# Kernel tuning notes

Hardware: AMD Instinct MI355X
Metric: run time of the kernel (lower is better)

The kernel has to match this reference:

```python
import jax, jax.numpy as jnp
import numpy as np
from jax import lax

EPS = 1e-5
DW_THRESH = 4.0
PW_THRESH = 1e-3


def setup_inputs() -> dict:
    key = jax.random.key(0)
    ks = jax.random.split(key, 13)
    B, C, O, H, W = 32, 256, 256, 56, 56
    inp = {
        "x": jax.random.normal(ks[0], (B, C, H, W), jnp.float32),
        "dw_w": jax.random.normal(ks[1], (C, 1, 3, 3), jnp.float32) * 0.2,
        "dw_b": jax.random.normal(ks[2], (C,), jnp.float32) * 0.1,
        "bn1_gamma": 0.5 + jax.random.uniform(ks[3], (C,), jnp.float32) * 1.5,
        "bn1_beta": jax.random.normal(ks[4], (C,), jnp.float32) * 0.5,
        "bn1_mean": jax.random.normal(ks[5], (C,), jnp.float32) * 0.1,
        "bn1_var": 0.5 + jax.random.uniform(ks[6], (C,), jnp.float32),
        "pw_w": jax.random.normal(ks[7], (O, C, 1, 1), jnp.float32) * 0.06,
        "pw_b": jax.random.normal(ks[8], (O,), jnp.float32) * 0.1,
        "bn2_gamma": 0.5 + jax.random.uniform(ks[9], (O,), jnp.float32) * 1.5,
        "bn2_beta": jax.random.normal(ks[10], (O,), jnp.float32) * 0.5,
        "bn2_mean": jax.random.normal(ks[11], (O,), jnp.float32) * 0.1,
        "bn2_var": 0.5 + jax.random.uniform(ks[12], (O,), jnp.float32),
    }
    return inp


def _bn(x, gamma, beta, mean, var):
    # inference-mode BatchNorm2d over channel axis 1
    inv = gamma * lax.rsqrt(var + EPS)
    return x * inv[None, :, None, None] + (beta - mean * inv)[None, :, None, None]


def _cut(x, thresh):
    # per-(batch, channel) max-abs pruning: max(max(x), -min(x)) == max(|x|)
    max_abs = jnp.max(jnp.abs(x), axis=(2, 3))  # [B, C]
    return jnp.where((max_abs < thresh)[:, :, None, None], 0.0, x)


def reference(x, dw_w, dw_b, bn1_gamma, bn1_beta, bn1_mean, bn1_var,
              pw_w, pw_b, bn2_gamma, bn2_beta, bn2_mean, bn2_var):
    C = x.shape[1]
    # depthwise 3x3 conv, padding=1, groups=C
    y = lax.conv_general_dilated(
        x, dw_w, window_strides=(1, 1), padding=[(1, 1), (1, 1)],
        feature_group_count=C,
        dimension_numbers=("NCHW", "OIHW", "NCHW"),
    ) + dw_b[None, :, None, None]
    y = jax.nn.relu(_bn(y, bn1_gamma, bn1_beta, bn1_mean, bn1_var))
    y = _cut(y, DW_THRESH)
    # pointwise 1x1 conv as channel contraction
    z = jnp.einsum("bihw,oi->bohw", y, pw_w[:, :, 0, 0]) + pw_b[None, :, None, None]
    z = jax.nn.relu(_bn(z, bn2_gamma, bn2_beta, bn2_mean, bn2_var))
    z = _cut(z, PW_THRESH)
    return z
```

## Files before the change

### kernel.cpp

```cpp
#include <hip/hip_runtime.h>
#include <hip/hip_bf16.h>
#include <stdint.h>

#define BATCH 32
#define CIN   256
#define COUT  256
#define HW    3136
#define NPAD  3200

typedef short bf16x8 __attribute__((ext_vector_type(8)));
typedef float f32x4  __attribute__((ext_vector_type(4)));

__device__ __forceinline__ unsigned short f2bf(float f) {
    unsigned u = __float_as_uint(f);
    u += 0x7fffu + ((u >> 16) & 1u);
    return (unsigned short)(u >> 16);
}

__global__ __launch_bounds__(256) void prep_kernel(
        const float* __restrict__ pw_w, const float* __restrict__ pw_b,
        const float* __restrict__ g2, const float* __restrict__ be2,
        const float* __restrict__ mu2, const float* __restrict__ va2,
        unsigned short* __restrict__ Wp, float* __restrict__ b2,
        unsigned* __restrict__ pwmax) {
    int o = blockIdx.x;
    int t = threadIdx.x;
    float inv2 = g2[o] * rsqrtf(va2[o] + 1e-5f);
    Wp[o * CIN + t] = f2bf(pw_w[o * CIN + t] * inv2);
    if (t == 0) b2[o] = pw_b[o] * inv2 + be2[o] - mu2[o] * inv2;
    int idx = blockIdx.x * 256 + t;
    if (idx < BATCH * COUT) pwmax[idx] = 0u;
}

#define LOADROW(dst, rp, mrow) do {                                        \
    float4 v0_ = *(const float4*)((rp) + c0);                              \
    float4 v1_ = *(const float4*)((rp) + c0 + 4);                          \
    dst[0] = (rp)[lidx] * (msL * (mrow));                                  \
    dst[1] = v0_.x * (mrow); dst[2] = v0_.y * (mrow);                      \
    dst[3] = v0_.z * (mrow); dst[4] = v0_.w * (mrow);                      \
    dst[5] = v1_.x * (mrow); dst[6] = v1_.y * (mrow);                      \
    dst[7] = v1_.z * (mrow); dst[8] = v1_.w * (mrow);                      \
    dst[9] = (rp)[ridx] * (msR * (mrow));                                  \
} while (0)

__global__ __launch_bounds__(256, 3) void dw_kernel(
        const float* __restrict__ x, const float* __restrict__ dww,
        const float* __restrict__ dwb,
        const float* __restrict__ g1, const float* __restrict__ be1,
        const float* __restrict__ mu1, const float* __restrict__ va1,
        unsigned short* __restrict__ y, float* __restrict__ dwmax) {
    int tid = threadIdx.x;
    int blk = blockIdx.x;
    __shared__ float lmx[256];

    float lmax = 0.f;
    if (tid < 224) {
        int p    = tid / 28;
        int r28  = tid - p * 28;
        int band = r28 / 7;
        int sc   = r28 - band * 7;
        int plane = blk * 8 + p;
        int c = plane & 255;
        int r0 = band * 14;
        int c0 = sc * 8;

        const float* xq = x + (size_t)plane * HW;
        float w00 = dww[c*9+0], w01 = dww[c*9+1], w02 = dww[c*9+2];
        float w10 = dww[c*9+3], w11 = dww[c*9+4], w12 = dww[c*9+5];
        float w20 = dww[c*9+6], w21 = dww[c*9+7], w22 = dww[c*9+8];
        float inv = g1[c] * rsqrtf(va1[c] + 1e-5f);
        float b0  = dwb[c] * inv + (be1[c] - mu1[c] * inv);

        float msL  = (sc == 0) ? 0.f : 1.f;
        float msR  = (sc == 6) ? 0.f : 1.f;
        int   lidx = (sc == 0) ? c0 : c0 - 1;
        int   ridx = (sc == 6) ? c0 + 7 : c0 + 8;
        float mTop = (band == 0) ? 0.f : 1.f;
        float mBot = (band == 3) ? 0.f : 1.f;

        float A[10], Bv[10], Cv[10], nx[10];
        {
            const float* rp = xq + ((band == 0) ? 0 : (r0 - 1)) * 56;
            LOADROW(A, rp, mTop);
        }
        {
            const float* rp = xq + r0 * 56;
            LOADROW(Bv, rp, 1.f);
        }
        {
            const float* rp = xq + (r0 + 1) * 56;
            LOADROW(nx, rp, 1.f);
        }
        unsigned short* yq = y + (size_t)plane * NPAD + c0;

#pragma unroll
        for (int i = 0; i < 14; ++i) {
#pragma unroll
            for (int t2 = 0; t2 < 10; ++t2) Cv[t2] = nx[t2];
            if (i < 13) {
                const float* rp = xq + ((i == 12) ? ((band == 3) ? 55 : (r0 + 14))
                                                  : (r0 + i + 2)) * 56;
                if (i == 12) { LOADROW(nx, rp, mBot); }
                else         { LOADROW(nx, rp, 1.f); }
            }
            unsigned us[8];
#pragma unroll
            for (int j = 0; j < 8; ++j) {
                float o = fmaf(A[j],    w00, fmaf(A[j+1],  w01, fmaf(A[j+2],  w02,
                          fmaf(Bv[j],   w10, fmaf(Bv[j+1], w11, fmaf(Bv[j+2], w12,
                          fmaf(Cv[j],   w20, fmaf(Cv[j+1], w21, Cv[j+2] * w22))))))));
                float v = fmaxf(fmaf(o, inv, b0), 0.f);
                lmax = fmaxf(lmax, v);
                us[j] = f2bf(v);
            }
            uint4 st;
            st.x = us[0] | (us[1] << 16);
            st.y = us[2] | (us[3] << 16);
            st.z = us[4] | (us[5] << 16);
            st.w = us[6] | (us[7] << 16);
            *(uint4*)(yq + (r0 + i) * 56) = st;
#pragma unroll
            for (int t2 = 0; t2 < 10; ++t2) { A[t2] = Bv[t2]; Bv[t2] = Cv[t2]; }
        }
    }
    lmx[tid] = lmax;
    __syncthreads();
    if (tid < 8) {
        float m = 0.f;
#pragma unroll 4
        for (int j = 0; j < 28; ++j) m = fmaxf(m, lmx[tid * 28 + j]);
        dwmax[blk * 8 + tid] = m;
    }
    if (tid < 64) {
        int p = tid >> 3;
        uint4* dst = (uint4*)(y + (size_t)(blk * 8 + p) * NPAD + HW) + (tid & 7);
        *dst = make_uint4(0, 0, 0, 0);
    }
}

__global__ __launch_bounds__(256) void pw_kernel(
        const unsigned short* __restrict__ y, const unsigned short* __restrict__ Wp,
        const float* __restrict__ b2, const float* __restrict__ dwm,
        float* __restrict__ z, unsigned* __restrict__ pwmax) {
    __shared__ __align__(16) unsigned short Al[128 * 64];
    __shared__ __align__(16) unsigned short Bl[128 * 64];

    int bid0 = blockIdx.x;
    int bid = (bid0 & 7) * 200 + (bid0 >> 3);
    int mt = bid & 1;
    int rest = bid >> 1;
    int nt = rest % 25;
    int b = rest / 25;
    int m0 = mt * 128, n0 = nt * 128;

    int tid = threadIdx.x;
    int lane = tid & 63, wid = tid >> 6;
    int wm = (wid & 1) * 64, wn = (wid >> 1) * 64;
    int l15 = lane & 15, l4 = lane >> 4;

    const unsigned short* yb = y + (size_t)b * CIN * NPAD;
    const float* dwb_ = dwm + b * 256;

    int am[4], acch[4];
    const unsigned short* asrc[4];
#pragma unroll
    for (int i = 0; i < 4; ++i) {
        int s = i * 256 + tid;
        int m = s >> 3, cch = s & 7, dch = cch ^ (m & 7);
        am[i] = m; acch[i] = cch;
        asrc[i] = Wp + (size_t)(m0 + m) * CIN + dch * 8;
    }
    int bq[2], bnq[2];
    const unsigned short* bsrc[2];
#pragma unroll
    for (int i = 0; i < 2; ++i) {
        int u = tid + i * 256;
        bq[i] = u >> 5; bnq[i] = u & 31;
        bsrc[i] = yb + (size_t)(bq[i] * 4) * NPAD + n0 + bnq[i] * 4;
    }

    uint4 areg[4];
    uint2 breg[2][4];
    float4 fl[2];
#pragma unroll
    for (int i = 0; i < 4; ++i) areg[i] = *(const uint4*)(asrc[i]);
#pragma unroll
    for (int i = 0; i < 2; ++i) {
#pragma unroll
        for (int r = 0; r < 4; ++r) breg[i][r] = *(const uint2*)(bsrc[i] + r * NPAD);
        fl[i] = *(const float4*)(dwb_ + bq[i] * 4);
    }

    f32x4 acc[4][4];
#pragma unroll
    for (int mf = 0; mf < 4; ++mf)
#pragma unroll
        for (int nf = 0; nf < 4; ++nf) acc[mf][nf] = {0.f, 0.f, 0.f, 0.f};

#pragma unroll
    for (int kk = 0; kk < 4; ++kk) {
        __builtin_amdgcn_s_barrier();
        __builtin_amdgcn_sched_barrier(0);
#pragma unroll
        for (int i = 0; i < 4; ++i)
            *(uint4*)((char*)Al + am[i] * 128 + acch[i] * 16) = areg[i];
#pragma unroll
        for (int i = 0; i < 2; ++i) {
            unsigned mk0 = fl[i].x >= 4.0f ? 0xffffffffu : 0u;
            unsigned mk1 = fl[i].y >= 4.0f ? 0xffffffffu : 0u;
            unsigned mk2 = fl[i].z >= 4.0f ? 0xffffffffu : 0u;
            unsigned mk3 = fl[i].w >= 4.0f ? 0xffffffffu : 0u;
            uint2 r0 = breg[i][0], r1 = breg[i][1], r2 = breg[i][2], r3 = breg[i][3];
            r0.x &= mk0; r0.y &= mk0; r1.x &= mk1; r1.y &= mk1;
            r2.x &= mk2; r2.y &= mk2; r3.x &= mk3; r3.y &= mk3;
            int q = bq[i], nq = bnq[i];
#pragma unroll
            for (int i2 = 0; i2 < 4; ++i2) {
                unsigned x0 = (i2 & 2) ? r0.y : r0.x;
                unsigned x1 = (i2 & 2) ? r1.y : r1.x;
                unsigned x2 = (i2 & 2) ? r2.y : r2.x;
                unsigned x3 = (i2 & 2) ? r3.y : r3.x;
                if (i2 & 1) { x0 >>= 16; x2 >>= 16; }
                else        { x0 &= 0xffffu; x2 &= 0xffffu; }
                unsigned px = (i2 & 1) ? (x0 | (x1 & 0xffff0000u))
                                       : (x0 | (x1 << 16));
                unsigned py = (i2 & 1) ? (x2 | (x3 & 0xffff0000u))
                                       : (x2 | (x3 << 16));
                int nloc = nq * 4 + i2;
                int sb = nloc * 128 + (((q >> 1) ^ ((nloc >> 2) & 7)) << 4) + ((q & 1) << 3);
                *(uint2*)((char*)Bl + sb) = make_uint2(px, py);
            }
        }
        if (kk < 3) {
#pragma unroll
            for (int i = 0; i < 4; ++i)
                areg[i] = *(const uint4*)(asrc[i] + (kk + 1) * 64);
#pragma unroll
            for (int i = 0; i < 2; ++i) {
#pragma unroll
                for (int r = 0; r < 4; ++r)
                    breg[i][r] = *(const uint2*)(bsrc[i] + (size_t)(kk + 1) * 64 * NPAD + r * NPAD);
                fl[i] = *(const float4*)(dwb_ + (kk + 1) * 64 + bq[i] * 4);
            }
        }
        asm volatile("s_waitcnt lgkmcnt(0)" ::: "memory");
        __builtin_amdgcn_s_barrier();
        __builtin_amdgcn_sched_barrier(0);
#pragma unroll
        for (int h = 0; h < 2; ++h) {
            bf16x8 af[4], bfr[4];
            int cc = h * 4 + l4;
#pragma unroll
            for (int mf = 0; mf < 4; ++mf) {
                int m = wm + mf * 16 + l15;
                af[mf] = *(const bf16x8*)((const char*)Al + m * 128 + ((cc ^ (m & 7)) << 4));
            }
#pragma unroll
            for (int nf = 0; nf < 4; ++nf) {
                int n = wn + nf * 16 + l15;
                bfr[nf] = *(const bf16x8*)((const char*)Bl + n * 128 + ((cc ^ ((n >> 2) & 7)) << 4));
            }
#pragma unroll
            for (int mf = 0; mf < 4; ++mf)
#pragma unroll
                for (int nf = 0; nf < 4; ++nf)
                    acc[mf][nf] = __builtin_amdgcn_mfma_f32_16x16x32_bf16(
                        af[mf], bfr[nf], acc[mf][nf], 0, 0, 0);
        }
    }

    float* zb = z + (size_t)b * COUT * HW;
#pragma unroll
    for (int mf = 0; mf < 4; ++mf) {
        int obase = m0 + wm + mf * 16 + l4 * 4;
        float bb0 = b2[obase + 0], bb1 = b2[obase + 1];
        float bb2v = b2[obase + 2], bb3 = b2[obase + 3];
        float rmax[4] = {0.f, 0.f, 0.f, 0.f};
#pragma unroll
        for (int nf = 0; nf < 4; ++nf) {
            int n = n0 + wn + nf * 16 + l15;
            bool valid = (n < HW);
            float v0 = fmaxf(acc[mf][nf][0] + bb0, 0.f);
            float v1 = fmaxf(acc[mf][nf][1] + bb1, 0.f);
            float v2 = fmaxf(acc[mf][nf][2] + bb2v, 0.f);
            float v3 = fmaxf(acc[mf][nf][3] + bb3, 0.f);
            if (valid) {
                zb[(size_t)(obase + 0) * HW + n] = v0;
                zb[(size_t)(obase + 1) * HW + n] = v1;
                zb[(size_t)(obase + 2) * HW + n] = v2;
                zb[(size_t)(obase + 3) * HW + n] = v3;
                rmax[0] = fmaxf(rmax[0], v0);
                rmax[1] = fmaxf(rmax[1], v1);
                rmax[2] = fmaxf(rmax[2], v2);
                rmax[3] = fmaxf(rmax[3], v3);
            }
        }
#pragma unroll
        for (int r = 0; r < 4; ++r) {
            float v = rmax[r];
            v = fmaxf(v, __shfl_xor(v, 1, 64));
            v = fmaxf(v, __shfl_xor(v, 2, 64));
            v = fmaxf(v, __shfl_xor(v, 4, 64));
            v = fmaxf(v, __shfl_xor(v, 8, 64));
            if (l15 == 0)
                atomicMax(&pwmax[b * COUT + obase + r], __float_as_uint(v));
        }
    }
}

__global__ __launch_bounds__(256) void cut_kernel(const unsigned* __restrict__ pwmax,
                                                  float* __restrict__ z) {
    int base = blockIdx.x * 8;
#pragma unroll
    for (int j = 0; j < 8; ++j) {
        int bo = base + j;
        if (__uint_as_float(pwmax[bo]) >= 1e-3f) continue;
        float4* zp = (float4*)(z + (size_t)bo * HW);
        for (int i = threadIdx.x; i < HW / 4; i += 256)
            zp[i] = make_float4(0.f, 0.f, 0.f, 0.f);
    }
}

extern "C" void kernel_launch(void* const* d_in, const int* in_sizes, int n_in,
                              void* d_out, int out_size, void* d_ws, size_t ws_size,
                              hipStream_t stream) {
    const float* x   = (const float*)d_in[0];
    const float* dww = (const float*)d_in[1];
    const float* dwb = (const float*)d_in[2];
    const float* g1  = (const float*)d_in[3];
    const float* be1 = (const float*)d_in[4];
    const float* mu1 = (const float*)d_in[5];
    const float* va1 = (const float*)d_in[6];
    const float* pww = (const float*)d_in[7];
    const float* pwb = (const float*)d_in[8];
    const float* g2  = (const float*)d_in[9];
    const float* be2 = (const float*)d_in[10];
    const float* mu2 = (const float*)d_in[11];
    const float* va2 = (const float*)d_in[12];
    float* z = (float*)d_out;

    char* ws = (char*)d_ws;
    const size_t Y_BYTES = (size_t)BATCH * CIN * NPAD * 2;
    unsigned short* y  = (unsigned short*)ws;
    unsigned short* Wp = (unsigned short*)(ws + Y_BYTES);
    float* b2          = (float*)(ws + Y_BYTES + 131072);
    unsigned* pwmax    = (unsigned*)(ws + Y_BYTES + 131072 + 1024);
    float* dwmax       = (float*)(ws + Y_BYTES + 131072 + 1024 + 32768);

    prep_kernel<<<256, 256, 0, stream>>>(pww, pwb, g2, be2, mu2, va2, Wp, b2, pwmax);
    dw_kernel<<<1024, 256, 0, stream>>>(x, dww, dwb, g1, be1, mu1, va1, y, dwmax);
    pw_kernel<<<1600, 256, 0, stream>>>(y, Wp, b2, dwmax, z, pwmax);
    cut_kernel<<<BATCH * COUT / 8, 256, 0, stream>>>(pwmax, z);
}
```

Measured before the change: 112.6 us.

## Deepen depthwise row prefetch and use hardware packed bf16 conversion

The depthwise kernel now keeps two rows in flight ahead of compute (N1/N2) instead of one, so global loads have more time to land before they are needed. The software round-to-nearest bf16 conversion is replaced with the v_cvt_pk_bf16_f32 instruction, and the per-element max is restructured into a pairwise tree. The launch-bounds occupancy hint of 3 is dropped to make room for the extra registers, at the cost of possibly lower occupancy.

```diff
diff --git a/kernel.cpp b/kernel.cpp
--- a/kernel.cpp
+++ b/kernel.cpp
@@ -32,18 +32,7 @@
     if (idx < BATCH * COUT) pwmax[idx] = 0u;
 }
 
-#define LOADROW(dst, rp, mrow) do {                                        \
-    float4 v0_ = *(const float4*)((rp) + c0);                              \
-    float4 v1_ = *(const float4*)((rp) + c0 + 4);                          \
-    dst[0] = (rp)[lidx] * (msL * (mrow));                                  \
-    dst[1] = v0_.x * (mrow); dst[2] = v0_.y * (mrow);                      \
-    dst[3] = v0_.z * (mrow); dst[4] = v0_.w * (mrow);                      \
-    dst[5] = v1_.x * (mrow); dst[6] = v1_.y * (mrow);                      \
-    dst[7] = v1_.z * (mrow); dst[8] = v1_.w * (mrow);                      \
-    dst[9] = (rp)[ridx] * (msR * (mrow));                                  \
-} while (0)
-
-__global__ __launch_bounds__(256, 3) void dw_kernel(
+__global__ __launch_bounds__(256) void dw_kernel(
         const float* __restrict__ x, const float* __restrict__ dww,
         const float* __restrict__ dwb,
         const float* __restrict__ g1, const float* __restrict__ be1,
@@ -78,50 +67,61 @@
         float mTop = (band == 0) ? 0.f : 1.f;
         float mBot = (band == 3) ? 0.f : 1.f;
 
-        float A[10], Bv[10], Cv[10], nx[10];
-        {
-            const float* rp = xq + ((band == 0) ? 0 : (r0 - 1)) * 56;
-            LOADROW(A, rp, mTop);
-        }
-        {
-            const float* rp = xq + r0 * 56;
-            LOADROW(Bv, rp, 1.f);
-        }
-        {
-            const float* rp = xq + (r0 + 1) * 56;
-            LOADROW(nx, rp, 1.f);
-        }
+        float A[10], Bv[10], Cv[10], N1[10], N2[10];
+
+#define LR(dst, q) do {                                                    \
+        const float* rp_ = xq + (q) * 56;                                  \
+        float4 u0_ = *(const float4*)(rp_ + c0);                           \
+        float4 u1_ = *(const float4*)(rp_ + c0 + 4);                       \
+        dst[0] = rp_[lidx] * msL;                                          \
+        dst[1] = u0_.x; dst[2] = u0_.y; dst[3] = u0_.z; dst[4] = u0_.w;    \
+        dst[5] = u1_.x; dst[6] = u1_.y; dst[7] = u1_.z; dst[8] = u1_.w;    \
+        dst[9] = rp_[ridx] * msR;                                          \
+} while (0)
+
+        LR(A, (band == 0) ? 0 : (r0 - 1));
+#pragma unroll
+        for (int t2 = 0; t2 < 10; ++t2) A[t2] *= mTop;
+        LR(Bv, r0);
+        LR(Cv, r0 + 1);
+        LR(N1, r0 + 2);
+        LR(N2, r0 + 3);
+
         unsigned short* yq = y + (size_t)plane * NPAD + c0;
 
 #pragma unroll
         for (int i = 0; i < 14; ++i) {
-#pragma unroll
-            for (int t2 = 0; t2 < 10; ++t2) Cv[t2] = nx[t2];
-            if (i < 13) {
-                const float* rp = xq + ((i == 12) ? ((band == 3) ? 55 : (r0 + 14))
-                                                  : (r0 + i + 2)) * 56;
-                if (i == 12) { LOADROW(nx, rp, mBot); }
-                else         { LOADROW(nx, rp, 1.f); }
-            }
-            unsigned us[8];
+            float v[8];
 #pragma unroll
             for (int j = 0; j < 8; ++j) {
                 float o = fmaf(A[j],    w00, fmaf(A[j+1],  w01, fmaf(A[j+2],  w02,
                           fmaf(Bv[j],   w10, fmaf(Bv[j+1], w11, fmaf(Bv[j+2], w12,
                           fmaf(Cv[j],   w20, fmaf(Cv[j+1], w21, Cv[j+2] * w22))))))));
-                float v = fmaxf(fmaf(o, inv, b0), 0.f);
-                lmax = fmaxf(lmax, v);
-                us[j] = f2bf(v);
-            }
+                v[j] = fmaxf(fmaf(o, inv, b0), 0.f);
+            }
+            lmax = fmaxf(lmax, fmaxf(v[0], v[1]));
+            lmax = fmaxf(lmax, fmaxf(v[2], v[3]));
+            lmax = fmaxf(lmax, fmaxf(v[4], v[5]));
+            lmax = fmaxf(lmax, fmaxf(v[6], v[7]));
             uint4 st;
-            st.x = us[0] | (us[1] << 16);
-            st.y = us[2] | (us[3] << 16);
-            st.z = us[4] | (us[5] << 16);
-            st.w = us[6] | (us[7] << 16);
+            asm("v_cvt_pk_bf16_f32 %0, %1, %2" : "=v"(st.x) : "v"(v[0]), "v"(v[1]));
+            asm("v_cvt_pk_bf16_f32 %0, %1, %2" : "=v"(st.y) : "v"(v[2]), "v"(v[3]));
+            asm("v_cvt_pk_bf16_f32 %0, %1, %2" : "=v"(st.z) : "v"(v[4]), "v"(v[5]));
+            asm("v_cvt_pk_bf16_f32 %0, %1, %2" : "=v"(st.w) : "v"(v[6]), "v"(v[7]));
             *(uint4*)(yq + (r0 + i) * 56) = st;
 #pragma unroll
-            for (int t2 = 0; t2 < 10; ++t2) { A[t2] = Bv[t2]; Bv[t2] = Cv[t2]; }
-        }
+            for (int t2 = 0; t2 < 10; ++t2) {
+                A[t2] = Bv[t2]; Bv[t2] = Cv[t2]; Cv[t2] = N1[t2]; N1[t2] = N2[t2];
+            }
+            if (i < 10) {
+                LR(N2, r0 + i + 4);
+            } else if (i == 10) {
+                LR(N2, (band == 3) ? 55 : (r0 + 14));
+#pragma unroll
+                for (int t2 = 0; t2 < 10; ++t2) N2[t2] *= mBot;
+            }
+        }
+#undef LR
     }
     lmx[tid] = lmax;
     __syncthreads();
```

Result: faster. 99.41 us (-11.7%).
